# Optimization experiments

Hardware: AMD Instinct MI355X
Metric: run time of the kernel (lower is better)

Reference implementation:

```python
import jax, jax.numpy as jnp
import numpy as np

T, B, IN, H, OUT = 2048, 64, 128, 256, 128


def setup_inputs() -> dict:
    key = jax.random.key(0)
    ks = jax.random.split(key, 7)
    s_ih = 1.0 / np.sqrt(H)
    return {
        "input": jax.random.normal(ks[0], (T, B, IN), dtype=jnp.float32),
        "W_ih": jax.random.uniform(ks[1], (4 * H, IN), minval=-s_ih, maxval=s_ih, dtype=jnp.float32),
        "W_hh": jax.random.uniform(ks[2], (4 * H, H), minval=-s_ih, maxval=s_ih, dtype=jnp.float32),
        "b_ih": jax.random.uniform(ks[3], (4 * H,), minval=-s_ih, maxval=s_ih, dtype=jnp.float32),
        "b_hh": jax.random.uniform(ks[4], (4 * H,), minval=-s_ih, maxval=s_ih, dtype=jnp.float32),
        "W_out": jax.random.uniform(ks[5], (OUT, H), minval=-s_ih, maxval=s_ih, dtype=jnp.float32),
        "b_out": jax.random.uniform(ks[6], (OUT,), minval=-s_ih, maxval=s_ih, dtype=jnp.float32),
    }


def reference(input, W_ih, W_hh, b_ih, b_hh, W_out, b_out):
    # input: [T, B, IN]. PyTorch LSTMCell gate order: i, f, g, o (chunks of H).
    H_ = W_hh.shape[1]
    # Precompute input-side gate pre-activations for all timesteps: [T, B, 4H]
    x_gates = jnp.einsum("tbi,gi->tbg", input, W_ih) + b_ih + b_hh

    def step(carry, xg):
        h, c = carry
        gates = xg + h @ W_hh.T  # [B, 4H]
        i = jax.nn.sigmoid(gates[:, 0 * H_:1 * H_])
        f = jax.nn.sigmoid(gates[:, 1 * H_:2 * H_])
        g = jnp.tanh(gates[:, 2 * H_:3 * H_])
        o = jax.nn.sigmoid(gates[:, 3 * H_:4 * H_])
        c_new = f * c + i * g
        h_new = o * jnp.tanh(c_new)
        y = h_new @ W_out.T + b_out  # [B, OUT]
        return (h_new, c_new), y

    Bsz = input.shape[1]
    h0 = jnp.zeros((Bsz, H_), dtype=input.dtype)
    c0 = jnp.zeros((Bsz, H_), dtype=input.dtype)
    (h_T, c_T), outputs = jax.lax.scan(step, (h0, c0), x_gates)
    return outputs, (h_T, c_T)
```

## Files before the change

kernel.cpp:

```cpp
#include <hip/hip_runtime.h>
#include <cstdint>
#include <cstddef>

#define TT   2048
#define BB   64
#define IND  128
#define HH   256
#define GG   1024
#define OUTD 128
#define TC   64
#define NCH  (TT / TC)

static const size_t XG0_OFF    = 0;
static const size_t XG1_OFF    = 8388608ull;
static const size_t HST0_OFF   = 16777216ull;
static const size_t HST1_OFF   = 18874368ull;
static const size_t WHH_OFF    = 20971520ull;
static const size_t WIH_OFF    = WHH_OFF  + 524288ull;
static const size_t WOUT_OFF   = WIH_OFF  + 262144ull;
static const size_t BSUM_OFF   = WOUT_OFF + 65536ull;
static const size_t HSTATE_OFF = BSUM_OFF + 4096ull;
static const size_t CSTATE_OFF = HSTATE_OFF + 32768ull;
static const size_t WS_NEEDED  = CSTATE_OFF + 65536ull;

static const int SMEM_SZ = 131072 + 1024;

typedef _Float16 h2 __attribute__((ext_vector_type(2)));

union U16 { uint4 u; h2 h[4]; };
union HU  { unsigned short u; _Float16 h; };

__device__ __forceinline__ float fdot2f(h2 a, h2 b, float c) {
#if __has_builtin(__builtin_amdgcn_fdot2)
  return __builtin_amdgcn_fdot2(a, b, c, false);
#else
  return c + (float)a.x * (float)b.x + (float)a.y * (float)b.y;
#endif
}

__device__ __forceinline__ float sigm(float x) { return 1.f / (1.f + __expf(-x)); }
__device__ __forceinline__ float tanh_fast(float x) {
  float ax = fabsf(x);
  float e  = __expf(-2.f * ax);
  float r  = (1.f - e) / (1.f + e);
  return x < 0.f ? -r : r;
}

__global__ void k0_pack(const float* __restrict__ Whh, const float* __restrict__ Wih,
                        const float* __restrict__ Wout, const float* __restrict__ bih,
                        const float* __restrict__ bhh, uint8_t* __restrict__ ws) {
  int tid = blockIdx.x * 256 + threadIdx.x;
  if (tid < 32768) {
    int rr = tid >> 13, rem = tid & 8191;
    int q = rem >> 9, u2 = rem & 511;
    int u = u2 >> 1, hf = u2 & 1;
    int row = (rr == 0) ? u : (rr == 1) ? 256 + u : (rr == 2) ? 768 + u : 512 + u;
    int kb = hf * 128 + q * 8;
    const float4* s = (const float4*)(Whh + (size_t)row * HH + kb);
    float4 v0 = s[0], v1 = s[1];
    U16 o;
    o.h[0].x = (_Float16)v0.x; o.h[0].y = (_Float16)v0.y;
    o.h[1].x = (_Float16)v0.z; o.h[1].y = (_Float16)v0.w;
    o.h[2].x = (_Float16)v1.x; o.h[2].y = (_Float16)v1.y;
    o.h[3].x = (_Float16)v1.z; o.h[3].y = (_Float16)v1.w;
    ((uint4*)(ws + WHH_OFF))[tid] = o.u;
  } else if (tid < 65536) {
    int t2 = tid - 32768;
    ((_Float16*)(ws + WOUT_OFF))[t2] = (_Float16)Wout[t2];
  } else if (tid < 81920) {
    int i = tid - 65536;
    const float4* s = (const float4*)(Wih + (size_t)i * 8);
    float4 v0 = s[0], v1 = s[1];
    U16 o;
    o.h[0].x = (_Float16)v0.x; o.h[0].y = (_Float16)v0.y;
    o.h[1].x = (_Float16)v0.z; o.h[1].y = (_Float16)v0.w;
    o.h[2].x = (_Float16)v1.x; o.h[2].y = (_Float16)v1.y;
    o.h[3].x = (_Float16)v1.z; o.h[3].y = (_Float16)v1.w;
    ((uint4*)(ws + WIH_OFF))[i] = o.u;
  } else if (tid < 82944) {
    int n = tid - 81920;
    ((float*)(ws + BSUM_OFF))[n] = bih[n] + bhh[n];
  }
}

__global__ void __launch_bounds__(256) k1_xgemm(const float* __restrict__ x,
                                                uint8_t* __restrict__ ws) {
  const uint4* Wp   = (const uint4*)(ws + WIH_OFF);
  const float* bsum = (const float*)(ws + BSUM_OFF);
  _Float16*    xg   = (_Float16*)(ws + XG0_OFF);

  const int s = blockIdx.x >> 4;
  const int m = ((blockIdx.x & 15) << 8) + threadIdx.x;

  __shared__ uint4 wlds[1024];
  __shared__ float bsl[64];
  #pragma unroll
  for (int i = 0; i < 4; ++i)
    wlds[i * 256 + threadIdx.x] = Wp[(size_t)(s << 6) * 16 + i * 256 + threadIdx.x];
  if (threadIdx.x < 64) bsl[threadIdx.x] = bsum[(s << 6) + threadIdx.x];
  __syncthreads();

  const float4* xr = (const float4*)(x + (size_t)m * IND);
  h2 xv[64];
  #pragma unroll
  for (int i = 0; i < 32; ++i) {
    float4 v = xr[i];
    xv[2*i  ].x = (_Float16)v.x; xv[2*i  ].y = (_Float16)v.y;
    xv[2*i+1].x = (_Float16)v.z; xv[2*i+1].y = (_Float16)v.w;
  }
  _Float16* xgrow = xg + (size_t)m * GG + (s << 6);
  for (int g = 0; g < 8; ++g) {
    float acc[8];
    #pragma unroll
    for (int j = 0; j < 8; ++j) {
      const uint4* wr = &wlds[(g * 8 + j) * 16];
      float a = bsl[g * 8 + j];
      #pragma unroll
      for (int q = 0; q < 16; ++q) {
        U16 w; w.u = wr[q];
        a = fdot2f(w.h[0], xv[4*q+0], a);
        a = fdot2f(w.h[1], xv[4*q+1], a);
        a = fdot2f(w.h[2], xv[4*q+2], a);
        a = fdot2f(w.h[3], xv[4*q+3], a);
      }
      acc[j] = a;
    }
    U16 o;
    #pragma unroll
    for (int p = 0; p < 4; ++p) { o.h[p].x = (_Float16)acc[2*p]; o.h[p].y = (_Float16)acc[2*p+1]; }
    *(uint4*)(xgrow + g * 8) = o.u;
  }
}

__global__ void __launch_bounds__(512)
__attribute__((amdgpu_waves_per_eu(2, 2)))
k2_fused(const float* __restrict__ x,
         uint8_t* __restrict__ ws,
         const float* __restrict__ b_out,
         float* __restrict__ out, int ch) {
  extern __shared__ __align__(16) uint8_t smem[];
  const int bi  = blockIdx.x;
  const int tid = threadIdx.x;

  if (bi < 64) {
    if (ch >= NCH) return;
    const int b    = bi;
    const int u    = tid >> 1;
    const int half = tid & 1;
    const int t0   = ch * TC;

    const uint4* WR = (const uint4*)(ws + WHH_OFF);
    const uint4* WG = WR + 24576;
    const unsigned short* xp = (const unsigned short*)(ws + ((ch & 1) ? XG1_OFF : XG0_OFF));
    _Float16* hst    = (_Float16*)(ws + ((ch & 1) ? HST1_OFF : HST0_OFF));
    _Float16* hstate = (_Float16*)(ws + HSTATE_OFF);
    float*    cstate = (float*)(ws + CSTATE_OFF);

    uint4*    gws   = (uint4*)smem;
    _Float16* h_lds = (_Float16*)(smem + 131072);

    h2 wi[64], wf[64], wo[64];
    #pragma unroll
    for (int q = 0; q < 16; ++q) {
      U16 a;
      a.u = WR[q * 512 + tid];
      wi[4*q+0]=a.h[0]; wi[4*q+1]=a.h[1]; wi[4*q+2]=a.h[2]; wi[4*q+3]=a.h[3];
      a.u = WR[8192 + q * 512 + tid];
      wf[4*q+0]=a.h[0]; wf[4*q+1]=a.h[1]; wf[4*q+2]=a.h[2]; wf[4*q+3]=a.h[3];
      a.u = WR[16384 + q * 512 + tid];
      wo[4*q+0]=a.h[0]; wo[4*q+1]=a.h[1]; wo[4*q+2]=a.h[2]; wo[4*q+3]=a.h[3];
    }
    #pragma unroll
    for (int j = 0; j < 16; ++j) gws[j * 512 + tid] = WG[j * 512 + tid];

    if (tid < 32) {
      uint4 z = make_uint4(0u, 0u, 0u, 0u);
      ((uint4*)h_lds)[tid] = (t0 == 0) ? z : ((const uint4*)(hstate + (size_t)b * HH))[tid];
    }
    float c = 0.f;
    if (t0 != 0) c = cstate[(size_t)b * HH + u];

    const size_t xrow = (size_t)b * GG;
    HU xi, xf, xgv, xo;
    xi.u  = xp[xrow + u];
    xf.u  = xp[xrow + 256 + u];
    xgv.u = xp[xrow + 512 + u];
    xo.u  = xp[xrow + 768 + u];
    __syncthreads();

    for (int tt = 0; tt < TC; ++tt) {
      float ai = 0.f, af = 0.f, ag = 0.f, ao = 0.f;
      const uint4* hv = ((const uint4*)h_lds) + (tt & 1) * 32 + half * 16;
      #pragma unroll
      for (int q = 0; q < 16; ++q) {
        U16 hh;  hh.u  = hv[q];
        U16 wg_; wg_.u = gws[q * 512 + tid];
        #pragma unroll
        for (int j = 0; j < 4; ++j) {
          ai = fdot2f(wi[4*q+j], hh.h[j], ai);
          af = fdot2f(wf[4*q+j], hh.h[j], af);
          ag = fdot2f(wg_.h[j],  hh.h[j], ag);
          ao = fdot2f(wo[4*q+j], hh.h[j], ao);
        }
      }
      ai += __shfl_xor(ai, 1);
      af += __shfl_xor(af, 1);
      ag += __shfl_xor(ag, 1);
      ao += __shfl_xor(ao, 1);
      float gi = sigm(ai + (float)xi.h);
      float gf = sigm(af + (float)xf.h);
      float gg = tanh_fast(ag + (float)xgv.h);
      float go = sigm(ao + (float)xo.h);
      c = gf * c + gi * gg;
      float hn = go * tanh_fast(c);
      if (half == 0) {
        h_lds[((tt + 1) & 1) * HH + u] = (_Float16)hn;
        hst[((size_t)tt * BB + b) * HH + u] = (_Float16)hn;
        if (t0 + tt == TT - 1) {
          const size_t tail = (size_t)TT * BB * OUTD;
          out[tail + (size_t)b * HH + u] = hn;
          out[tail + (size_t)BB * HH + (size_t)b * HH + u] = c;
        }
      }
      if (tt + 1 < TC) {
        const size_t nx = xrow + (size_t)(tt + 1) * (BB * GG);
        xi.u  = xp[nx + u];
        xf.u  = xp[nx + 256 + u];
        xgv.u = xp[nx + 512 + u];
        xo.u  = xp[nx + 768 + u];
      }
      __syncthreads();
    }

    if (tid < 32) ((uint4*)(hstate + (size_t)b * HH))[tid] = ((const uint4*)h_lds)[tid];
    if (half == 0) cstate[(size_t)b * HH + u] = c;

  } else if (bi < 192) {
    if (ch + 1 >= NCH) return;
    const int p    = bi - 64;
    const int seg  = p >> 3;
    const int rowg = p & 7;
    const int m    = rowg * 512 + tid;
    const int t0n  = (ch + 1) * TC;

    const uint4* Wp   = (const uint4*)(ws + WIH_OFF);
    const float* bsum = (const float*)(ws + BSUM_OFF);
    _Float16*    xgn  = (_Float16*)(ws + (((ch + 1) & 1) ? XG1_OFF : XG0_OFF));

    uint4* wlds = (uint4*)smem;
    float* bsl  = (float*)(smem + 16384);
    wlds[tid]       = Wp[(size_t)(seg << 6) * 16 + tid];
    wlds[tid + 512] = Wp[(size_t)(seg << 6) * 16 + 512 + tid];
    if (tid < 64) bsl[tid] = bsum[(seg << 6) + tid];
    __syncthreads();

    const float4* xr = (const float4*)(x + ((size_t)t0n * BB + m) * IND);
    h2 xv[64];
    #pragma unroll
    for (int i = 0; i < 32; ++i) {
      float4 v = xr[i];
      xv[2*i  ].x = (_Float16)v.x; xv[2*i  ].y = (_Float16)v.y;
      xv[2*i+1].x = (_Float16)v.z; xv[2*i+1].y = (_Float16)v.w;
    }
    _Float16* xgrow = xgn + (size_t)m * GG + (seg << 6);
    for (int g = 0; g < 8; ++g) {
      float acc[8];
      #pragma unroll
      for (int j = 0; j < 8; ++j) {
        const uint4* wr = &wlds[(g * 8 + j) * 16];
        float a = bsl[g * 8 + j];
        #pragma unroll
        for (int q = 0; q < 16; ++q) {
          U16 w; w.u = wr[q];
          a = fdot2f(w.h[0], xv[4*q+0], a);
          a = fdot2f(w.h[1], xv[4*q+1], a);
          a = fdot2f(w.h[2], xv[4*q+2], a);
          a = fdot2f(w.h[3], xv[4*q+3], a);
        }
        acc[j] = a;
      }
      U16 o;
      #pragma unroll
      for (int pk = 0; pk < 4; ++pk) { o.h[pk].x = (_Float16)acc[2*pk]; o.h[pk].y = (_Float16)acc[2*pk+1]; }
      *(uint4*)(xgrow + g * 8) = o.u;
    }

  } else {
    if (ch < 1) return;
    const int yb   = bi - 192;
    const int seg  = yb & 15;
    const int rowg = yb >> 4;
    const int t0p  = (ch - 1) * TC;

    const _Float16* hstp = (const _Float16*)(ws + (((ch - 1) & 1) ? HST1_OFF : HST0_OFF));
    const uint4* WO = (const uint4*)(ws + WOUT_OFF);

    uint4* wlds = (uint4*)smem;
    float* bsl  = (float*)(smem + 4096);
    if (tid < 256) wlds[tid] = WO[(size_t)(seg * 8) * 32 + tid];
    if (tid < 8)   bsl[tid]  = b_out[seg * 8 + tid];
    __syncthreads();

    #pragma unroll
    for (int rr = 0; rr < 4; ++rr) {
      const int r = rowg * 2048 + rr * 512 + tid;
      const uint4* hr = (const uint4*)(hstp + (size_t)r * HH);
      float acc[8];
      #pragma unroll
      for (int j = 0; j < 8; ++j) acc[j] = bsl[j];
      #pragma unroll 4
      for (int q = 0; q < 32; ++q) {
        U16 hh; hh.u = hr[q];
        #pragma unroll
        for (int j = 0; j < 8; ++j) {
          U16 w; w.u = wlds[j * 32 + q];
          acc[j] = fdot2f(w.h[0], hh.h[0], acc[j]);
          acc[j] = fdot2f(w.h[1], hh.h[1], acc[j]);
          acc[j] = fdot2f(w.h[2], hh.h[2], acc[j]);
          acc[j] = fdot2f(w.h[3], hh.h[3], acc[j]);
        }
      }
      float* orow = out + ((size_t)t0p * BB + r) * OUTD + seg * 8;
      *(float4*)(orow)     = make_float4(acc[0], acc[1], acc[2], acc[3]);
      *(float4*)(orow + 4) = make_float4(acc[4], acc[5], acc[6], acc[7]);
    }
  }
}

extern "C" void kernel_launch(void* const* d_in, const int* in_sizes, int n_in,
                              void* d_out, int out_size, void* d_ws, size_t ws_size,
                              hipStream_t stream) {
  const float* input = (const float*)d_in[0];
  const float* W_ih  = (const float*)d_in[1];
  const float* W_hh  = (const float*)d_in[2];
  const float* b_ih  = (const float*)d_in[3];
  const float* b_hh  = (const float*)d_in[4];
  const float* W_out = (const float*)d_in[5];
  const float* b_out = (const float*)d_in[6];
  float*   out = (float*)d_out;
  uint8_t* ws  = (uint8_t*)d_ws;

  if (ws_size < WS_NEEDED) return;

  hipFuncSetAttribute((const void*)k2_fused,
                      hipFuncAttributeMaxDynamicSharedMemorySize, SMEM_SZ);

  hipLaunchKernelGGL(k0_pack,  dim3(324), dim3(256), 0, stream,
                     W_hh, W_ih, W_out, b_ih, b_hh, ws);
  hipLaunchKernelGGL(k1_xgemm, dim3(256), dim3(256), 0, stream, input, ws);
  for (int ch = 0; ch <= NCH; ++ch) {
    hipLaunchKernelGGL(k2_fused, dim3(224), dim3(512), SMEM_SZ, stream,
                       input, ws, b_out, out, ch);
  }
}
```

Before: 3.735 ms.

## Use 1024-thread blocks with four lanes per hidden unit in recurrence

The recurrent blocks now run 1024 threads, so each hidden unit's dot product is split over four lanes instead of two. This halves per-thread register weights and serial FMA chain length, at the cost of an extra shuffle-reduction stage. The side projection blocks are remapped to fewer, larger blocks to match the new block size. The waves-per-EU hint is dropped, so register pressure and occupancy are now left to the compiler.

```diff
diff --git a/kernel.cpp b/kernel.cpp
--- a/kernel.cpp
+++ b/kernel.cpp
@@ -132,8 +132,7 @@
   }
 }
 
-__global__ void __launch_bounds__(512)
-__attribute__((amdgpu_waves_per_eu(2, 2)))
+__global__ void __launch_bounds__(1024)
 k2_fused(const float* __restrict__ x,
          uint8_t* __restrict__ ws,
          const float* __restrict__ b_out,
@@ -145,8 +144,10 @@
   if (bi < 64) {
     if (ch >= NCH) return;
     const int b    = bi;
-    const int u    = tid >> 1;
-    const int half = tid & 1;
+    const int u    = tid >> 2;
+    const int qk   = tid & 3;
+    const int u2g  = (u << 1) + (qk >> 1);
+    const int qoff = (qk & 1) << 3;
     const int t0   = ch * TC;
 
     const uint4* WR = (const uint4*)(ws + WHH_OFF);
@@ -159,19 +160,19 @@
     uint4*    gws   = (uint4*)smem;
     _Float16* h_lds = (_Float16*)(smem + 131072);
 
-    h2 wi[64], wf[64], wo[64];
-    #pragma unroll
-    for (int q = 0; q < 16; ++q) {
+    h2 wi[32], wf[32], wo[32];
+    #pragma unroll
+    for (int j = 0; j < 8; ++j) {
       U16 a;
-      a.u = WR[q * 512 + tid];
-      wi[4*q+0]=a.h[0]; wi[4*q+1]=a.h[1]; wi[4*q+2]=a.h[2]; wi[4*q+3]=a.h[3];
-      a.u = WR[8192 + q * 512 + tid];
-      wf[4*q+0]=a.h[0]; wf[4*q+1]=a.h[1]; wf[4*q+2]=a.h[2]; wf[4*q+3]=a.h[3];
-      a.u = WR[16384 + q * 512 + tid];
-      wo[4*q+0]=a.h[0]; wo[4*q+1]=a.h[1]; wo[4*q+2]=a.h[2]; wo[4*q+3]=a.h[3];
-    }
-    #pragma unroll
-    for (int j = 0; j < 16; ++j) gws[j * 512 + tid] = WG[j * 512 + tid];
+      a.u = WR[(qoff + j) * 512 + u2g];
+      wi[4*j+0]=a.h[0]; wi[4*j+1]=a.h[1]; wi[4*j+2]=a.h[2]; wi[4*j+3]=a.h[3];
+      a.u = WR[8192 + (qoff + j) * 512 + u2g];
+      wf[4*j+0]=a.h[0]; wf[4*j+1]=a.h[1]; wf[4*j+2]=a.h[2]; wf[4*j+3]=a.h[3];
+      a.u = WR[16384 + (qoff + j) * 512 + u2g];
+      wo[4*j+0]=a.h[0]; wo[4*j+1]=a.h[1]; wo[4*j+2]=a.h[2]; wo[4*j+3]=a.h[3];
+    }
+    #pragma unroll
+    for (int j = 0; j < 8; ++j) gws[j * 1024 + tid] = WG[j * 1024 + tid];
 
     if (tid < 32) {
       uint4 z = make_uint4(0u, 0u, 0u, 0u);
@@ -190,30 +191,30 @@
 
     for (int tt = 0; tt < TC; ++tt) {
       float ai = 0.f, af = 0.f, ag = 0.f, ao = 0.f;
-      const uint4* hv = ((const uint4*)h_lds) + (tt & 1) * 32 + half * 16;
-      #pragma unroll
-      for (int q = 0; q < 16; ++q) {
-        U16 hh;  hh.u  = hv[q];
-        U16 wg_; wg_.u = gws[q * 512 + tid];
+      const uint4* hv = ((const uint4*)h_lds) + (tt & 1) * 32 + qk * 8;
+      #pragma unroll
+      for (int j = 0; j < 8; ++j) {
+        U16 hh;  hh.u  = hv[j];
+        U16 wg_; wg_.u = gws[(qoff + j) * 512 + u2g];
         #pragma unroll
-        for (int j = 0; j < 4; ++j) {
-          ai = fdot2f(wi[4*q+j], hh.h[j], ai);
-          af = fdot2f(wf[4*q+j], hh.h[j], af);
-          ag = fdot2f(wg_.h[j],  hh.h[j], ag);
-          ao = fdot2f(wo[4*q+j], hh.h[j], ao);
+        for (int jj = 0; jj < 4; ++jj) {
+          ai = fdot2f(wi[4*j+jj], hh.h[jj], ai);
+          af = fdot2f(wf[4*j+jj], hh.h[jj], af);
+          ag = fdot2f(wg_.h[jj],  hh.h[jj], ag);
+          ao = fdot2f(wo[4*j+jj], hh.h[jj], ao);
         }
       }
-      ai += __shfl_xor(ai, 1);
-      af += __shfl_xor(af, 1);
-      ag += __shfl_xor(ag, 1);
-      ao += __shfl_xor(ao, 1);
+      ai += __shfl_xor(ai, 1); ai += __shfl_xor(ai, 2);
+      af += __shfl_xor(af, 1); af += __shfl_xor(af, 2);
+      ag += __shfl_xor(ag, 1); ag += __shfl_xor(ag, 2);
+      ao += __shfl_xor(ao, 1); ao += __shfl_xor(ao, 2);
       float gi = sigm(ai + (float)xi.h);
       float gf = sigm(af + (float)xf.h);
       float gg = tanh_fast(ag + (float)xgv.h);
       float go = sigm(ao + (float)xo.h);
       c = gf * c + gi * gg;
       float hn = go * tanh_fast(c);
-      if (half == 0) {
+      if (qk == 0) {
         h_lds[((tt + 1) & 1) * HH + u] = (_Float16)hn;
         hst[((size_t)tt * BB + b) * HH + u] = (_Float16)hn;
         if (t0 + tt == TT - 1) {
@@ -233,14 +234,14 @@
     }
 
     if (tid < 32) ((uint4*)(hstate + (size_t)b * HH))[tid] = ((const uint4*)h_lds)[tid];
-    if (half == 0) cstate[(size_t)b * HH + u] = c;
-
-  } else if (bi < 192) {
+    if (qk == 0) cstate[(size_t)b * HH + u] = c;
+
+  } else if (bi < 128) {
     if (ch + 1 >= NCH) return;
     const int p    = bi - 64;
-    const int seg  = p >> 3;
-    const int rowg = p & 7;
-    const int m    = rowg * 512 + tid;
+    const int seg  = p >> 2;
+    const int rowg = p & 3;
+    const int m    = rowg * 1024 + tid;
     const int t0n  = (ch + 1) * TC;
 
     const uint4* Wp   = (const uint4*)(ws + WIH_OFF);
@@ -249,8 +250,7 @@
 
     uint4* wlds = (uint4*)smem;
     float* bsl  = (float*)(smem + 16384);
-    wlds[tid]       = Wp[(size_t)(seg << 6) * 16 + tid];
-    wlds[tid + 512] = Wp[(size_t)(seg << 6) * 16 + 512 + tid];
+    wlds[tid] = Wp[(size_t)seg * 1024 + tid];
     if (tid < 64) bsl[tid] = bsum[(seg << 6) + tid];
     __syncthreads();
 
@@ -287,9 +287,7 @@
 
   } else {
     if (ch < 1) return;
-    const int yb   = bi - 192;
-    const int seg  = yb & 15;
-    const int rowg = yb >> 4;
+    const int seg  = bi - 128;
     const int t0p  = (ch - 1) * TC;
 
     const _Float16* hstp = (const _Float16*)(ws + (((ch - 1) & 1) ? HST1_OFF : HST0_OFF));
@@ -303,7 +301,7 @@
 
     #pragma unroll
     for (int rr = 0; rr < 4; ++rr) {
-      const int r = rowg * 2048 + rr * 512 + tid;
+      const int r = rr * 1024 + tid;
       const uint4* hr = (const uint4*)(hstp + (size_t)r * HH);
       float acc[8];
       #pragma unroll
@@ -349,7 +347,7 @@
                      W_hh, W_ih, W_out, b_ih, b_hh, ws);
   hipLaunchKernelGGL(k1_xgemm, dim3(256), dim3(256), 0, stream, input, ws);
   for (int ch = 0; ch <= NCH; ++ch) {
-    hipLaunchKernelGGL(k2_fused, dim3(224), dim3(512), SMEM_SZ, stream,
+    hipLaunchKernelGGL(k2_fused, dim3(144), dim3(1024), SMEM_SZ, stream,
                        input, ws, b_out, out, ch);
   }
 }
```

Measured after the change: 5.348 ms. 1.43x slower.
